# Optimization experiments

Measured on AMD Instinct MI355X. Metric: run time of the kernel, lower is better.

Reference implementation:

```python
import jax, jax.numpy as jnp
import numpy as np

N = 100_000      # nodes
E = 1_600_000    # edges
F_IN = 128       # n_features == conv_dim1..3
F_OUT = 256      # concat_dim
G = 2000         # number of graphs in the batch
EPS = 1e-5       # BatchNorm eps


def _xavier(k, shape):
    fan_in, fan_out = shape[-2], shape[-1]
    lim = float(np.sqrt(6.0 / (fan_in + fan_out)))
    return jax.random.uniform(k, shape, jnp.float32, -lim, lim)


def setup_inputs() -> dict:
    key = jax.random.key(0)
    ks = jax.random.split(key, 8)
    x = jax.random.normal(ks[0], (N, F_IN), jnp.float32)
    edge_index = jax.random.randint(ks[1], (2, E), 0, N, dtype=jnp.int64)
    batch = jnp.sort(jax.random.randint(ks[2], (N,), 0, G, dtype=jnp.int64))
    # layers 1..5: F_IN -> F_IN (stacked), layer 6: F_IN -> F_OUT
    Wi = _xavier(ks[3], (5, F_IN, F_IN))   # ARMA init_weight per layer
    Wr = _xavier(ks[4], (5, F_IN, F_IN))   # ARMA root_weight per layer
    b = jnp.zeros((5, F_IN), jnp.float32)  # ARMA bias per layer
    g = jnp.ones((5, F_IN), jnp.float32)   # BN gamma
    be = jnp.zeros((5, F_IN), jnp.float32) # BN beta
    Wi6 = _xavier(ks[5], (F_IN, F_OUT))
    Wr6 = _xavier(ks[6], (F_IN, F_OUT))
    b6 = jnp.zeros((F_OUT,), jnp.float32)
    g6 = jnp.ones((F_OUT,), jnp.float32)
    be6 = jnp.zeros((F_OUT,), jnp.float32)
    return dict(x=x, edge_index=edge_index, batch=batch, Wi=Wi, Wr=Wr, b=b,
                g=g, be=be, Wi6=Wi6, Wr6=Wr6, b6=b6, g6=g6, be6=be6)


def _arma(x, norm, row, col, Wi_l, Wr_l, b_l):
    # ARMAConv (num_stacks=1, num_layers=1, act=ReLU):
    #   out = ReLU( A_norm @ (x W_init) + x W_root + b )
    h = x @ Wi_l                                           # [N, F_out]
    msg = h[row] * norm[:, None]                           # gather + scale, [E, F_out]
    agg = jax.ops.segment_sum(msg, col, num_segments=N)    # scatter-add
    return jax.nn.relu(agg + x @ Wr_l + b_l)


def _bn(x, gamma, beta):
    # BatchNorm1d, training mode (biased batch variance)
    mu = x.mean(axis=0)
    var = x.var(axis=0)
    return gamma * (x - mu) * jax.lax.rsqrt(var + EPS) + beta


def reference(x, edge_index, batch, Wi, Wr, b, g, be, Wi6, Wr6, b6, g6, be6):
    row, col = edge_index[0], edge_index[1]
    # gcn_norm without self loops: D^-1/2 A D^-1/2 edge weights
    deg = jax.ops.segment_sum(jnp.ones((E,), x.dtype), col, num_segments=N)
    dinv = jnp.where(deg > 0, jax.lax.rsqrt(deg), 0.0)
    norm = dinv[row] * dinv[col]                           # [E]

    h = x
    for l in range(5):  # fixed small layer count
        h = _arma(h, norm, row, col, Wi[l], Wr[l], b[l])   # outer F.relu is idempotent
        h = _bn(h, g[l], be[l])
    h = _arma(h, norm, row, col, Wi6, Wr6, b6)
    h = _bn(h, g6, be6)
    # global_add_pool over graph ids; dropout = identity (deterministic baseline)
    out = jax.ops.segment_sum(h, batch, num_segments=G)    # [G, F_OUT]
    return out
```

## Files before the change

kernel.cpp:

```cpp
#include <hip/hip_runtime.h>

#define Nn 100000
#define NP 100001
#define Ee 1600000
#define Gg 2000
#define EPSf 1e-5f

typedef unsigned short ushort_t;
typedef __attribute__((ext_vector_type(8))) short short8;
typedef __attribute__((ext_vector_type(4))) float f32x4;
typedef __attribute__((ext_vector_type(4))) unsigned u32x4;

__device__ inline float bf2f(unsigned int u) {
    union { unsigned int i; float f; } v; v.i = u << 16; return v.f;
}
__device__ inline unsigned short f2bf(float f) {
    unsigned int x = __float_as_uint(f);
    unsigned int r = (x + 0x7fffu + ((x >> 16) & 1u)) >> 16;
    return (unsigned short)r;
}
__device__ inline int ldidx(const void* a, int i, int i64) {
    return i64 ? (int)((const long long*)a)[i] : ((const int*)a)[i];
}
__device__ inline float ldflt(const void* p, long long i, int f32) {
    return f32 ? ((const float*)p)[i] : bf2f(((const ushort_t*)p)[i]);
}


__global__ void k_flags(const void* gones, const void* ei, int* flags) {
    if (threadIdx.x == 0 && blockIdx.x == 0) {
        unsigned w = *(const unsigned*)gones;
        flags[0] = (w == 0x3F800000u) ? 1 : 0;
        const int* e = (const int*)ei;
        int nz = 0;
        for (int i = 0; i < 256; i++) nz |= e[2 * i + 1];
        flags[1] = nz ? 0 : 1;
    }
}


__global__ void k_hist(const void* __restrict__ ei, int* __restrict__ deg, const int* __restrict__ flags) {
    int i = blockIdx.x * 256 + threadIdx.x;
    if (i < Ee) {
        int c = ldidx(ei, Ee + i, flags[1]);
        atomicAdd(&deg[c], 1);
    }
}

__global__ void k_dinv(const int* __restrict__ deg, float* __restrict__ dinv) {
    int i = blockIdx.x * 256 + threadIdx.x;
    if (i < Nn) { int d = deg[i]; dinv[i] = d > 0 ? rsqrtf((float)d) : 0.f; }
}

__global__ void k_scan1(const int* __restrict__ deg, int* __restrict__ off, int* __restrict__ part) {
    __shared__ int sh[1024];
    int i = blockIdx.x * 1024 + threadIdx.x;
    int v = (i < Nn) ? ((deg[i] + 3) & ~3) : 0;
    sh[threadIdx.x] = v;
    __syncthreads();
    for (int ofs = 1; ofs < 1024; ofs <<= 1) {
        int t = 0;
        if ((int)threadIdx.x >= ofs) t = sh[threadIdx.x - ofs];
        __syncthreads();
        sh[threadIdx.x] += t;
        __syncthreads();
    }
    if (i < Nn) off[i] = sh[threadIdx.x] - v;
    if (threadIdx.x == 1023) part[blockIdx.x] = sh[1023];
}

__global__ void k_scan2(int* part, int nb) {
    if (threadIdx.x == 0 && blockIdx.x == 0) {
        int run = 0;
        for (int i = 0; i < nb; i++) { int t = part[i]; part[i] = run; run += t; }
        part[nb] = run;
    }
}

__global__ void k_scan3(int* __restrict__ off, const int* __restrict__ part, int* __restrict__ cursor) {
    int i = blockIdx.x * 256 + threadIdx.x;
    if (i < Nn) {
        int v = off[i] + part[i >> 10];
        off[i] = v;
        cursor[i] = v;
    }
    if (i == 0) off[Nn] = part[98];
}

__global__ void k_fillp(const void* __restrict__ ei, int* __restrict__ cursor,
                        int* __restrict__ srcS, const int* __restrict__ flags) {
    int range = blockIdx.x & 7;
    int e = (blockIdx.x >> 3) * 256 + threadIdx.x;
    if (e < Ee) {
        int i64 = flags[1];
        int c = ldidx(ei, Ee + e, i64);
        if (c >= range * 12500 && c < (range + 1) * 12500) {
            int r = ldidx(ei, e, i64);
            int p = atomicAdd(&cursor[c], 1);
            srcS[p] = r;
        }
    }
}

__global__ void k_pad(const int* __restrict__ cursor, const int* __restrict__ off,
                      int* __restrict__ srcS) {
    int i = blockIdx.x * 256 + threadIdx.x;
    if (i < Nn) {
        int e = off[i + 1];
        for (int p = cursor[i]; p < e; p++) srcS[p] = Nn;
    }
}

__global__ void k_zrow(ushort_t* __restrict__ Hi) {
    int t = threadIdx.x;
    int fc = t >> 4, j = t & 15;
    Hi[((size_t)fc * NP + Nn) * 16 + j] = 0;
}

__global__ void k_cvtp(const void* b, const void* b6, const void* g, const void* g6,
                       const void* be, const void* be6,
                       float* __restrict__ biasF, float* __restrict__ gF,
                       float* __restrict__ beF, const int* __restrict__ flags) {
    int i = blockIdx.x * 256 + threadIdx.x;
    if (i >= 2688) return;
    int grp = i / 896, r = i - grp * 896;
    int f32 = flags[0];
    const void* srcs[6] = { b, b6, g, g6, be, be6 };
    float* dsts[3] = { biasF, gF, beF };
    const void* s = (r < 640) ? srcs[grp * 2] : srcs[grp * 2 + 1];
    int idx = (r < 640) ? r : r - 640;
    dsts[grp][r] = ldflt(s, idx, f32);
}

__global__ void k_cvtx(const void* __restrict__ x, ushort_t* __restrict__ xq, const int* __restrict__ flags) {
    int node = blockIdx.x * 256 + threadIdx.x;
    int fc = blockIdx.y;
    if (node < Nn) {
        union { ushort_t u[16]; u32x4 v[2]; } t;
        if (flags[0]) {
            const float* p = (const float*)x + (size_t)node * 128 + fc * 16;
#pragma unroll
            for (int j = 0; j < 16; j++) t.u[j] = f2bf(p[j]);
        } else {
            const ushort_t* p = (const ushort_t*)x + (size_t)node * 128 + fc * 16;
#pragma unroll
            for (int j = 0; j < 16; j++) t.u[j] = p[j];
        }
        u32x4* d = (u32x4*)(xq + ((size_t)fc * Nn + node) * 16);
        d[0] = t.v[0]; d[1] = t.v[1];
    }
}

__global__ void k_pack(const void* __restrict__ Wi, const void* __restrict__ Wr,
                       const void* __restrict__ Wi6, const void* __restrict__ Wr6,
                       ushort_t* __restrict__ Bp, const int* __restrict__ flags) {
    int idx = blockIdx.x * 256 + threadIdx.x;
    if (idx >= 229376) return;
    int f32 = flags[0];
    if (idx < 163840) {
        int l = idx / 32768, rem = idx - l * 32768;
        int kg = rem / 2048, rem2 = rem - kg * 2048;
        int n = rem2 / 8, j = rem2 - n * 8;
        int k = kg * 8 + j;
        float v = (n < 128) ? ldflt(Wi, (l * 128 + k) * 128 + n, f32)
                            : ldflt(Wr, (l * 128 + k) * 128 + (n - 128), f32);
        Bp[idx] = f2bf(v);
    } else {
        int idx2 = idx - 163840;
        int kg = idx2 / 4096, rem2 = idx2 - kg * 4096;
        int n = rem2 / 8, j = rem2 - n * 8;
        int k = kg * 8 + j;
        float v = (n < 256) ? ldflt(Wi6, k * 256 + n, f32) : ldflt(Wr6, k * 256 + (n - 256), f32);
        Bp[idx] = f2bf(v);
    }
}

__global__ void k_fold(const ushort_t* __restrict__ Bp, const float* __restrict__ stat,
                       const float* __restrict__ gamma, const float* __restrict__ beta,
                       const float* __restrict__ bias,
                       ushort_t* __restrict__ Bp2, float* __restrict__ hcorr, int ncat) {
    __shared__ float red[128];
    int n = blockIdx.x, k = threadIdx.x;
    int fhalf = ncat >> 1;
    float mu = stat[k] * (1.f / Nn);
    float var = stat[128 + k] * (1.f / Nn) - mu * mu;
    float rs = rsqrtf(var + EPSf);
    float s = gamma[k] * rs;
    float h = beta[k] - s * mu;
    size_t idx = ((size_t)(k >> 3) * ncat + n) * 8 + (k & 7);
    float w = bf2f(Bp[idx]);
    Bp2[idx] = f2bf(w * s);
    red[k] = h * w;
    __syncthreads();
    for (int m = 64; m > 0; m >>= 1) { if (k < m) red[k] += red[k + m]; __syncthreads(); }
    if (k == 0) hcorr[n] = red[0] + (n >= fhalf ? bias[n - fhalf] : 0.f);
}

__global__ void k_h0(const float* __restrict__ bias, float* __restrict__ hc, int ncat) {
    int n = blockIdx.x * 256 + threadIdx.x;
    if (n < ncat) hc[n] = n >= (ncat >> 1) ? bias[n - (ncat >> 1)] : 0.f;
}


__global__ __launch_bounds__(256) void k_gemm(
        const ushort_t* __restrict__ Aq,
        const ushort_t* __restrict__ Bp, const float* __restrict__ hcorr,
        const float* __restrict__ dinv,
        ushort_t* __restrict__ Hi, ushort_t* __restrict__ yq, int ncat) {
    __shared__ ushort_t As[8448];
    const int tid = threadIdx.x, lane = tid & 63, wid = tid >> 6;
    const int row0 = blockIdx.x * 64;
    const int fhalf = ncat >> 1;

    {
        int node = row0 + lane;
#pragma unroll
        for (int i = 0; i < 4; i++) {
            int kg = wid * 4 + i;
            short8 t;
            if (node < Nn)
                t = *(const short8*)(Aq + ((size_t)(kg >> 1) * Nn + node) * 16 + (kg & 1) * 8);
            else {
#pragma unroll
                for (int j = 0; j < 8; j++) ((ushort_t*)&t)[j] = 0;
            }
            *(short8*)&As[(kg * 64 + lane) * 8] = t;
        }
    }
    __syncthreads();

    const int q = lane >> 4, l15 = lane & 15;
    const int wcL = wid * 64;

    f32x4 acc[4][4];
    f32x4 z; z.x = 0.f; z.y = 0.f; z.z = 0.f; z.w = 0.f;
#pragma unroll
    for (int rt = 0; rt < 4; rt++)
#pragma unroll
        for (int ct = 0; ct < 4; ct++) acc[rt][ct] = z;

#pragma unroll
    for (int kk = 0; kk < 4; kk++) {
        short8 af[4], bfr[4];
        int kg = kk * 4 + q;
#pragma unroll
        for (int rt = 0; rt < 4; rt++)
            af[rt] = *(const short8*)&As[((kg * 64) + rt * 16 + l15) * 8];
#pragma unroll
        for (int ct = 0; ct < 4; ct++) {
            int n = blockIdx.y * 256 + wcL + ct * 16 + l15;
            bfr[ct] = *(const short8*)(Bp + ((size_t)kg * ncat + n) * 8);
        }
#pragma unroll
        for (int rt = 0; rt < 4; rt++)
#pragma unroll
            for (int ct = 0; ct < 4; ct++)
                acc[rt][ct] = __builtin_amdgcn_mfma_f32_16x16x32_bf16(af[rt], bfr[ct], acc[rt][ct], 0, 0, 0);
    }

    ushort_t* stage = As;
#pragma unroll
    for (int half = 0; half < 2; half++) {
        __syncthreads();
#pragma unroll
        for (int ct = 0; ct < 4; ct++) {
            int lcol = wcL + ct * 16 + l15;
            int gcol = blockIdx.y * 256 + lcol;
            float hc = hcorr[gcol];
            bool isHi = gcol < fhalf;
#pragma unroll
            for (int rt2 = 0; rt2 < 2; rt2++) {
                int rt = half * 2 + rt2;
#pragma unroll
                for (int r = 0; r < 4; r++) {
                    int grow = row0 + rt * 16 + q * 4 + r;
                    int gr = grow < Nn ? grow : 0;
                    float v = acc[rt][ct][r] + hc;
                    if (isHi) v *= dinv[gr];
                    stage[(rt2 * 16 + q * 4 + r) * 264 + lcol] = f2bf(v);
                }
            }
        }
        __syncthreads();
        for (int chunk = tid; chunk < 512; chunk += 256) {
            int cg = chunk & 15, rl = chunk >> 4;
            int node = row0 + half * 32 + rl;
            if (node < Nn) {
                int gc0 = blockIdx.y * 256 + cg * 16;
                const u32x4* sp = (const u32x4*)&stage[rl * 264 + cg * 16];
                u32x4 v0 = sp[0], v1 = sp[1];
                ushort_t* dst = (gc0 < fhalf)
                    ? Hi + ((size_t)(gc0 >> 4) * NP + node) * 16
                    : yq + ((size_t)((gc0 - fhalf) >> 4) * Nn + node) * 16;
                u32x4* dp = (u32x4*)dst;
                dp[0] = v0; dp[1] = v1;
            }
        }
    }
}


__global__ __launch_bounds__(256) void k_agg8(const int* __restrict__ off, const int* __restrict__ src,
                                              const float* __restrict__ dinv, const unsigned* __restrict__ Hi2,
                                              unsigned* __restrict__ yq, float* __restrict__ stat,
                                              int F, int fcbase) {
    const int tid = threadIdx.x;
    const int w = tid >> 6, lane = tid & 63;
    const int sub = lane >> 3, fl = lane & 7;
    const int fc = fcbase + (blockIdx.x & 7);
    const int T = blockIdx.x >> 3;
    const unsigned* __restrict__ base = Hi2 + (size_t)fc * (NP * 8) + fl;
    float st0 = 0.f, st1 = 0.f, st2 = 0.f, st3 = 0.f;

#pragma unroll
    for (int pass = 0; pass < 4; pass++) {
        int node = T * 128 + pass * 32 + w * 8 + sub;
        bool valid = node < Nn;
        int p0 = 0, p1 = 0;
        if (valid) { p0 = off[node]; p1 = off[node + 1]; }
        float a0 = 0.f, a1 = 0.f;
        int p = p0;
        for (; p + 7 < p1; p += 8) {
            int4 sv0 = *(const int4*)(src + p);
            int4 sv1 = *(const int4*)(src + p + 4);
            unsigned u0 = base[(unsigned)sv0.x * 8u];
            unsigned u1 = base[(unsigned)sv0.y * 8u];
            unsigned u2 = base[(unsigned)sv0.z * 8u];
            unsigned u3 = base[(unsigned)sv0.w * 8u];
            unsigned u4 = base[(unsigned)sv1.x * 8u];
            unsigned u5 = base[(unsigned)sv1.y * 8u];
            unsigned u6 = base[(unsigned)sv1.z * 8u];
            unsigned u7 = base[(unsigned)sv1.w * 8u];
            a0 += bf2f(u0 & 0xffffu); a1 += bf2f(u0 >> 16);
            a0 += bf2f(u1 & 0xffffu); a1 += bf2f(u1 >> 16);
            a0 += bf2f(u2 & 0xffffu); a1 += bf2f(u2 >> 16);
            a0 += bf2f(u3 & 0xffffu); a1 += bf2f(u3 >> 16);
            a0 += bf2f(u4 & 0xffffu); a1 += bf2f(u4 >> 16);
            a0 += bf2f(u5 & 0xffffu); a1 += bf2f(u5 >> 16);
            a0 += bf2f(u6 & 0xffffu); a1 += bf2f(u6 >> 16);
            a0 += bf2f(u7 & 0xffffu); a1 += bf2f(u7 >> 16);
        }
        if (p < p1) {
            int4 sv0 = *(const int4*)(src + p);
            unsigned u0 = base[(unsigned)sv0.x * 8u];
            unsigned u1 = base[(unsigned)sv0.y * 8u];
            unsigned u2 = base[(unsigned)sv0.z * 8u];
            unsigned u3 = base[(unsigned)sv0.w * 8u];
            a0 += bf2f(u0 & 0xffffu); a1 += bf2f(u0 >> 16);
            a0 += bf2f(u1 & 0xffffu); a1 += bf2f(u1 >> 16);
            a0 += bf2f(u2 & 0xffffu); a1 += bf2f(u2 >> 16);
            a0 += bf2f(u3 & 0xffffu); a1 += bf2f(u3 >> 16);
        }
        if (valid) {
            float dv = dinv[node];
            unsigned* yp = yq + ((size_t)fc * Nn + node) * 8 + fl;
            unsigned uv = *yp;
            float vx = fmaxf(bf2f(uv & 0xffffu) + dv * a0, 0.f);
            float vy = fmaxf(bf2f(uv >> 16) + dv * a1, 0.f);
            *yp = (unsigned)f2bf(vx) | ((unsigned)f2bf(vy) << 16);
            st0 += vx; st1 += vx * vx;
            st2 += vy; st3 += vy * vy;
        }
    }
#pragma unroll
    for (int m = 8; m <= 32; m <<= 1) {
        st0 += __shfl_xor(st0, m, 64);
        st1 += __shfl_xor(st1, m, 64);
        st2 += __shfl_xor(st2, m, 64);
        st3 += __shfl_xor(st3, m, 64);
    }
    __shared__ float red[4][8][4];
    if (sub == 0) {
        red[w][fl][0] = st0; red[w][fl][1] = st1;
        red[w][fl][2] = st2; red[w][fl][3] = st3;
    }
    __syncthreads();
    if (tid < 32) {
        int rfl = tid >> 2, k = tid & 3;
        float s = red[0][rfl][k] + red[1][rfl][k] + red[2][rfl][k] + red[3][rfl][k];
        int f = fc * 16 + rfl * 2 + (k >> 1);
        atomicAdd(&stat[(k & 1) * F + f], s);
    }
}


__device__ inline int lb(const void* a, int n, int key, int i64) {
    int lo = 0, hi = n;
    while (lo < hi) { int mid = (lo + hi) >> 1; if (ldidx(a, mid, i64) < key) lo = mid + 1; else hi = mid; }
    return lo;
}

__global__ void k_pool(const ushort_t* __restrict__ y6q, const float* __restrict__ stat,
                       const float* __restrict__ g6, const float* __restrict__ be6,
                       const void* __restrict__ batch, void* __restrict__ out,
                       const int* __restrict__ flags) {
    int g = blockIdx.x;
    int f = threadIdx.x;
    int i64 = flags[1];
    int start = lb(batch, Nn, g, i64);
    int end = lb(batch, Nn, g + 1, i64);
    const ushort_t* yp = y6q + (size_t)(f >> 4) * Nn * 16 + (f & 15);
    float s = 0.f;
    for (int n = start; n < end; n++) s += bf2f(yp[(size_t)n * 16]);
    int cnt = end - start;
    float mu = stat[f] * (1.f / Nn);
    float var = stat[256 + f] * (1.f / Nn) - mu * mu;
    float rs = rsqrtf(var + EPSf);
    float val = g6[f] * rs * (s - (float)cnt * mu) + (float)cnt * be6[f];
    if (flags[0]) ((float*)out)[(size_t)g * 256 + f] = val;
    else          ((ushort_t*)out)[(size_t)g * 256 + f] = f2bf(val);
}


extern "C" void kernel_launch(void* const* d_in, const int* in_sizes, int n_in,
                              void* d_out, int out_size, void* d_ws, size_t ws_size,
                              hipStream_t stream) {
    const void* x    = d_in[0];
    const void* ei   = d_in[1];
    const void* batch= d_in[2];
    const void* Wi   = d_in[3];
    const void* Wr   = d_in[4];
    const void* b    = d_in[5];
    const void* g    = d_in[6];
    const void* be   = d_in[7];
    const void* Wi6  = d_in[8];
    const void* Wr6  = d_in[9];
    const void* b6   = d_in[10];
    const void* g6   = d_in[11];
    const void* be6  = d_in[12];

    char* p = (char*)d_ws;
    auto alloc = [&](size_t bytes) { char* r = p; p += (bytes + 511) & ~(size_t)511; return r; };
    ushort_t* HiB  = (ushort_t*)alloc((size_t)NP * 256 * 2);
    ushort_t* xq   = (ushort_t*)alloc((size_t)Nn * 128 * 2);
    ushort_t* yAq  = (ushort_t*)alloc((size_t)Nn * 128 * 2);
    ushort_t* yBq  = (ushort_t*)alloc((size_t)Nn * 128 * 2);
    ushort_t* y6q  = (ushort_t*)alloc((size_t)Nn * 256 * 2);
    int* srcS      = (int*)alloc(((size_t)Ee + 4 * Nn + 64) * 4);
    int* off       = (int*)alloc((size_t)(Nn + 1) * 4);
    int* cursor    = (int*)alloc((size_t)Nn * 4);
    int* deg       = (int*)alloc((size_t)Nn * 4);
    float* dinv    = (float*)alloc((size_t)Nn * 4);
    int* part      = (int*)alloc(128 * 4);
    float* statsA  = (float*)alloc(6 * 512 * 4);
    ushort_t* Bp   = (ushort_t*)alloc(229376 * 2);
    ushort_t* Bp2  = (ushort_t*)alloc(65536 * 2);
    float* hcorrA  = (float*)alloc(512 * 4);
    int* flags     = (int*)alloc(2 * 4);
    float* biasF   = (float*)alloc(896 * 4);
    float* gF      = (float*)alloc(896 * 4);
    float* beF     = (float*)alloc(896 * 4);
    const unsigned* Hi2 = (const unsigned*)HiB;

    const int AGG_GRID = 782 * 8;

    k_flags<<<1, 64, 0, stream>>>(g, ei, flags);
    k_cvtp<<<11, 256, 0, stream>>>(b, b6, g, g6, be, be6, biasF, gF, beF, flags);

    hipMemsetAsync(deg, 0, (size_t)Nn * 4, stream);
    hipMemsetAsync(statsA, 0, 6 * 512 * 4, stream);
    k_hist<<<6250, 256, 0, stream>>>(ei, deg, flags);
    k_dinv<<<391, 256, 0, stream>>>(deg, dinv);
    k_scan1<<<98, 1024, 0, stream>>>(deg, off, part);
    k_scan2<<<1, 64, 0, stream>>>(part, 98);
    k_scan3<<<391, 256, 0, stream>>>(off, part, cursor);
    k_fillp<<<50000, 256, 0, stream>>>(ei, cursor, srcS, flags);
    k_pad<<<391, 256, 0, stream>>>(cursor, off, srcS);
    k_zrow<<<1, 256, 0, stream>>>(HiB);
    k_pack<<<896, 256, 0, stream>>>(Wi, Wr, Wi6, Wr6, Bp, flags);
    k_cvtx<<<dim3(391, 8), 256, 0, stream>>>(x, xq, flags);
    k_h0<<<1, 256, 0, stream>>>(biasF, hcorrA, 256);

    k_gemm<<<dim3(1563, 1), 256, 0, stream>>>(xq, Bp, hcorrA, dinv, HiB, yAq, 256);
    k_agg8<<<AGG_GRID, 256, 0, stream>>>(off, srcS, dinv, Hi2, (unsigned*)yAq, statsA, 128, 0);
    k_fold<<<256, 128, 0, stream>>>(Bp + 32768, statsA, gF, beF, biasF + 128, Bp2, hcorrA, 256);

    k_gemm<<<dim3(1563, 1), 256, 0, stream>>>(yAq, Bp2, hcorrA, dinv, HiB, yBq, 256);
    k_agg8<<<AGG_GRID, 256, 0, stream>>>(off, srcS, dinv, Hi2, (unsigned*)yBq, statsA + 512, 128, 0);
    k_fold<<<256, 128, 0, stream>>>(Bp + 65536, statsA + 512, gF + 128, beF + 128, biasF + 256, Bp2, hcorrA, 256);

    k_gemm<<<dim3(1563, 1), 256, 0, stream>>>(yBq, Bp2, hcorrA, dinv, HiB, yAq, 256);
    k_agg8<<<AGG_GRID, 256, 0, stream>>>(off, srcS, dinv, Hi2, (unsigned*)yAq, statsA + 1024, 128, 0);
    k_fold<<<256, 128, 0, stream>>>(Bp + 98304, statsA + 1024, gF + 256, beF + 256, biasF + 384, Bp2, hcorrA, 256);

    k_gemm<<<dim3(1563, 1), 256, 0, stream>>>(yAq, Bp2, hcorrA, dinv, HiB, yBq, 256);
    k_agg8<<<AGG_GRID, 256, 0, stream>>>(off, srcS, dinv, Hi2, (unsigned*)yBq, statsA + 1536, 128, 0);
    k_fold<<<256, 128, 0, stream>>>(Bp + 131072, statsA + 1536, gF + 384, beF + 384, biasF + 512, Bp2, hcorrA, 256);

    k_gemm<<<dim3(1563, 1), 256, 0, stream>>>(yBq, Bp2, hcorrA, dinv, HiB, yAq, 256);
    k_agg8<<<AGG_GRID, 256, 0, stream>>>(off, srcS, dinv, Hi2, (unsigned*)yAq, statsA + 2048, 128, 0);
    k_fold<<<512, 128, 0, stream>>>(Bp + 163840, statsA + 2048, gF + 512, beF + 512, biasF + 640, Bp2, hcorrA, 512);

    k_gemm<<<dim3(1563, 2), 256, 0, stream>>>(yAq, Bp2, hcorrA, dinv, HiB, y6q, 512);
    k_agg8<<<AGG_GRID, 256, 0, stream>>>(off, srcS, dinv, Hi2, (unsigned*)y6q, statsA + 2560, 256, 0);
    k_agg8<<<AGG_GRID, 256, 0, stream>>>(off, srcS, dinv, Hi2, (unsigned*)y6q, statsA + 2560, 256, 8);
    k_pool<<<Gg, 256, 0, stream>>>(y6q, statsA + 2560, gF + 640, beF + 640, batch, d_out, flags);
}
```

Baseline: 1.165 ms.

## Make GEMM persistent over row tiles with register-resident B, unroll aggregation loop

```diff
diff --git a/kernel.cpp b/kernel.cpp
--- a/kernel.cpp
+++ b/kernel.cpp
@@ -207,93 +207,87 @@
         const ushort_t* __restrict__ Bp, const float* __restrict__ hcorr,
         const float* __restrict__ dinv,
         ushort_t* __restrict__ Hi, ushort_t* __restrict__ yq, int ncat) {
-    __shared__ ushort_t As[8448];
+    __shared__ ushort_t stage[32 * 264];
     const int tid = threadIdx.x, lane = tid & 63, wid = tid >> 6;
-    const int row0 = blockIdx.x * 64;
+    const int q = lane >> 4, l15 = lane & 15;
     const int fhalf = ncat >> 1;
-
-    {
-        int node = row0 + lane;
-#pragma unroll
-        for (int i = 0; i < 4; i++) {
-            int kg = wid * 4 + i;
-            short8 t;
-            if (node < Nn)
-                t = *(const short8*)(Aq + ((size_t)(kg >> 1) * Nn + node) * 16 + (kg & 1) * 8);
-            else {
-#pragma unroll
-                for (int j = 0; j < 8; j++) ((ushort_t*)&t)[j] = 0;
+    const int colW = blockIdx.y * 256 + wid * 64;
+
+    short8 bfr[4][4];
+    float hc[4];
+#pragma unroll
+    for (int kk = 0; kk < 4; kk++) {
+        int kg = kk * 4 + q;
+#pragma unroll
+        for (int ct = 0; ct < 4; ct++)
+            bfr[kk][ct] = *(const short8*)(Bp + ((size_t)kg * ncat + colW + ct * 16 + l15) * 8);
+    }
+#pragma unroll
+    for (int ct = 0; ct < 4; ct++) hc[ct] = hcorr[colW + ct * 16 + l15];
+
+    for (int t = 0; t < 4; t++) {
+        int row0 = (blockIdx.x * 4 + t) * 64;
+        if (row0 >= Nn) break;
+
+        f32x4 acc[4][4];
+        f32x4 z; z.x = 0.f; z.y = 0.f; z.z = 0.f; z.w = 0.f;
+#pragma unroll
+        for (int rt = 0; rt < 4; rt++)
+#pragma unroll
+            for (int ct = 0; ct < 4; ct++) acc[rt][ct] = z;
+
+#pragma unroll
+        for (int kk = 0; kk < 4; kk++) {
+            int kg = kk * 4 + q;
+            const ushort_t* ap = Aq + (size_t)(kg >> 1) * Nn * 16 + (kg & 1) * 8;
+            short8 af[4];
+#pragma unroll
+            for (int rt = 0; rt < 4; rt++) {
+                int node = row0 + rt * 16 + l15;
+                if (node >= Nn) node = Nn - 1;
+                af[rt] = *(const short8*)(ap + (size_t)node * 16);
             }
-            *(short8*)&As[(kg * 64 + lane) * 8] = t;
-        }
-    }
-    __syncthreads();
-
-    const int q = lane >> 4, l15 = lane & 15;
-    const int wcL = wid * 64;
-
-    f32x4 acc[4][4];
-    f32x4 z; z.x = 0.f; z.y = 0.f; z.z = 0.f; z.w = 0.f;
-#pragma unroll
-    for (int rt = 0; rt < 4; rt++)
-#pragma unroll
-        for (int ct = 0; ct < 4; ct++) acc[rt][ct] = z;
-
-#pragma unroll
-    for (int kk = 0; kk < 4; kk++) {
-        short8 af[4], bfr[4];
-        int kg = kk * 4 + q;
-#pragma unroll
-        for (int rt = 0; rt < 4; rt++)
-            af[rt] = *(const short8*)&As[((kg * 64) + rt * 16 + l15) * 8];
-#pragma unroll
-        for (int ct = 0; ct < 4; ct++) {
-            int n = blockIdx.y * 256 + wcL + ct * 16 + l15;
-            bfr[ct] = *(const short8*)(Bp + ((size_t)kg * ncat + n) * 8);
-        }
-#pragma unroll
-        for (int rt = 0; rt < 4; rt++)
-#pragma unroll
-            for (int ct = 0; ct < 4; ct++)
-                acc[rt][ct] = __builtin_amdgcn_mfma_f32_16x16x32_bf16(af[rt], bfr[ct], acc[rt][ct], 0, 0, 0);
-    }
-
-    ushort_t* stage = As;
-#pragma unroll
-    for (int half = 0; half < 2; half++) {
-        __syncthreads();
-#pragma unroll
-        for (int ct = 0; ct < 4; ct++) {
-            int lcol = wcL + ct * 16 + l15;
-            int gcol = blockIdx.y * 256 + lcol;
-            float hc = hcorr[gcol];
-            bool isHi = gcol < fhalf;
-#pragma unroll
-            for (int rt2 = 0; rt2 < 2; rt2++) {
-                int rt = half * 2 + rt2;
-#pragma unroll
-                for (int r = 0; r < 4; r++) {
-                    int grow = row0 + rt * 16 + q * 4 + r;
-                    int gr = grow < Nn ? grow : 0;
-                    float v = acc[rt][ct][r] + hc;
-                    if (isHi) v *= dinv[gr];
-                    stage[(rt2 * 16 + q * 4 + r) * 264 + lcol] = f2bf(v);
+#pragma unroll
+            for (int rt = 0; rt < 4; rt++)
+#pragma unroll
+                for (int ct = 0; ct < 4; ct++)
+                    acc[rt][ct] = __builtin_amdgcn_mfma_f32_16x16x32_bf16(af[rt], bfr[kk][ct], acc[rt][ct], 0, 0, 0);
+        }
+
+#pragma unroll
+        for (int half = 0; half < 2; half++) {
+            __syncthreads();
+#pragma unroll
+            for (int ct = 0; ct < 4; ct++) {
+                int lcol = wid * 64 + ct * 16 + l15;
+                bool isHi = (blockIdx.y * 256 + lcol) < fhalf;
+#pragma unroll
+                for (int rt2 = 0; rt2 < 2; rt2++) {
+                    int rt = half * 2 + rt2;
+#pragma unroll
+                    for (int r = 0; r < 4; r++) {
+                        int grow = row0 + rt * 16 + q * 4 + r;
+                        int gr = grow < Nn ? grow : 0;
+                        float v = acc[rt][ct][r] + hc[ct];
+                        if (isHi) v *= dinv[gr];
+                        stage[(rt2 * 16 + q * 4 + r) * 264 + lcol] = f2bf(v);
+                    }
                 }
             }
-        }
-        __syncthreads();
-        for (int chunk = tid; chunk < 512; chunk += 256) {
-            int cg = chunk & 15, rl = chunk >> 4;
-            int node = row0 + half * 32 + rl;
-            if (node < Nn) {
-                int gc0 = blockIdx.y * 256 + cg * 16;
-                const u32x4* sp = (const u32x4*)&stage[rl * 264 + cg * 16];
-                u32x4 v0 = sp[0], v1 = sp[1];
-                ushort_t* dst = (gc0 < fhalf)
-                    ? Hi + ((size_t)(gc0 >> 4) * NP + node) * 16
-                    : yq + ((size_t)((gc0 - fhalf) >> 4) * Nn + node) * 16;
-                u32x4* dp = (u32x4*)dst;
-                dp[0] = v0; dp[1] = v1;
+            __syncthreads();
+            for (int chunk = tid; chunk < 512; chunk += 256) {
+                int cg = chunk & 15, rl = chunk >> 4;
+                int node = row0 + half * 32 + rl;
+                if (node < Nn) {
+                    int gc0 = blockIdx.y * 256 + cg * 16;
+                    const u32x4* sp = (const u32x4*)&stage[rl * 264 + cg * 16];
+                    u32x4 v0 = sp[0], v1 = sp[1];
+                    ushort_t* dst = (gc0 < fhalf)
+                        ? Hi + ((size_t)(gc0 >> 4) * NP + node) * 16
+                        : yq + ((size_t)((gc0 - fhalf) >> 4) * Nn + node) * 16;
+                    u32x4* dp = (u32x4*)dst;
+                    dp[0] = v0; dp[1] = v1;
+                }
             }
         }
     }
@@ -320,17 +314,27 @@
         if (valid) { p0 = off[node]; p1 = off[node + 1]; }
         float a0 = 0.f, a1 = 0.f;
         int p = p0;
-        for (; p + 7 < p1; p += 8) {
-            int4 sv0 = *(const int4*)(src + p);
-            int4 sv1 = *(const int4*)(src + p + 4);
-            unsigned u0 = base[(unsigned)sv0.x * 8u];
-            unsigned u1 = base[(unsigned)sv0.y * 8u];
-            unsigned u2 = base[(unsigned)sv0.z * 8u];
-            unsigned u3 = base[(unsigned)sv0.w * 8u];
-            unsigned u4 = base[(unsigned)sv1.x * 8u];
-            unsigned u5 = base[(unsigned)sv1.y * 8u];
-            unsigned u6 = base[(unsigned)sv1.z * 8u];
-            unsigned u7 = base[(unsigned)sv1.w * 8u];
+        for (; p + 15 < p1; p += 16) {
+            int4 sa = *(const int4*)(src + p);
+            int4 sb = *(const int4*)(src + p + 4);
+            int4 sc = *(const int4*)(src + p + 8);
+            int4 sd = *(const int4*)(src + p + 12);
+            unsigned u0 = base[(unsigned)sa.x * 8u];
+            unsigned u1 = base[(unsigned)sa.y * 8u];
+            unsigned u2 = base[(unsigned)sa.z * 8u];
+            unsigned u3 = base[(unsigned)sa.w * 8u];
+            unsigned u4 = base[(unsigned)sb.x * 8u];
+            unsigned u5 = base[(unsigned)sb.y * 8u];
+            unsigned u6 = base[(unsigned)sb.z * 8u];
+            unsigned u7 = base[(unsigned)sb.w * 8u];
+            unsigned u8 = base[(unsigned)sc.x * 8u];
+            unsigned u9 = base[(unsigned)sc.y * 8u];
+            unsigned uA = base[(unsigned)sc.z * 8u];
+            unsigned uB = base[(unsigned)sc.w * 8u];
+            unsigned uC = base[(unsigned)sd.x * 8u];
+            unsigned uD = base[(unsigned)sd.y * 8u];
+            unsigned uE = base[(unsigned)sd.z * 8u];
+            unsigned uF = base[(unsigned)sd.w * 8u];
             a0 += bf2f(u0 & 0xffffu); a1 += bf2f(u0 >> 16);
             a0 += bf2f(u1 & 0xffffu); a1 += bf2f(u1 >> 16);
             a0 += bf2f(u2 & 0xffffu); a1 += bf2f(u2 >> 16);
@@ -339,13 +343,41 @@
             a0 += bf2f(u5 & 0xffffu); a1 += bf2f(u5 >> 16);
             a0 += bf2f(u6 & 0xffffu); a1 += bf2f(u6 >> 16);
             a0 += bf2f(u7 & 0xffffu); a1 += bf2f(u7 >> 16);
+            a0 += bf2f(u8 & 0xffffu); a1 += bf2f(u8 >> 16);
+            a0 += bf2f(u9 & 0xffffu); a1 += bf2f(u9 >> 16);
+            a0 += bf2f(uA & 0xffffu); a1 += bf2f(uA >> 16);
+            a0 += bf2f(uB & 0xffffu); a1 += bf2f(uB >> 16);
+            a0 += bf2f(uC & 0xffffu); a1 += bf2f(uC >> 16);
+            a0 += bf2f(uD & 0xffffu); a1 += bf2f(uD >> 16);
+            a0 += bf2f(uE & 0xffffu); a1 += bf2f(uE >> 16);
+            a0 += bf2f(uF & 0xffffu); a1 += bf2f(uF >> 16);
+        }
+        for (; p + 7 < p1; p += 8) {
+            int4 sa = *(const int4*)(src + p);
+            int4 sb = *(const int4*)(src + p + 4);
+            unsigned u0 = base[(unsigned)sa.x * 8u];
+            unsigned u1 = base[(unsigned)sa.y * 8u];
+            unsigned u2 = base[(unsigned)sa.z * 8u];
+            unsigned u3 = base[(unsigned)sa.w * 8u];
+            unsigned u4 = base[(unsigned)sb.x * 8u];
+            unsigned u5 = base[(unsigned)sb.y * 8u];
+            unsigned u6 = base[(unsigned)sb.z * 8u];
+            unsigned u7 = base[(unsigned)sb.w * 8u];
+            a0 += bf2f(u0 & 0xffffu); a1 += bf2f(u0 >> 16);
+            a0 += bf2f(u1 & 0xffffu); a1 += bf2f(u1 >> 16);
+            a0 += bf2f(u2 & 0xffffu); a1 += bf2f(u2 >> 16);
+            a0 += bf2f(u3 & 0xffffu); a1 += bf2f(u3 >> 16);
+            a0 += bf2f(u4 & 0xffffu); a1 += bf2f(u4 >> 16);
+            a0 += bf2f(u5 & 0xffffu); a1 += bf2f(u5 >> 16);
+            a0 += bf2f(u6 & 0xffffu); a1 += bf2f(u6 >> 16);
+            a0 += bf2f(u7 & 0xffffu); a1 += bf2f(u7 >> 16);
         }
         if (p < p1) {
-            int4 sv0 = *(const int4*)(src + p);
-            unsigned u0 = base[(unsigned)sv0.x * 8u];
-            unsigned u1 = base[(unsigned)sv0.y * 8u];
-            unsigned u2 = base[(unsigned)sv0.z * 8u];
-            unsigned u3 = base[(unsigned)sv0.w * 8u];
+            int4 sa = *(const int4*)(src + p);
+            unsigned u0 = base[(unsigned)sa.x * 8u];
+            unsigned u1 = base[(unsigned)sa.y * 8u];
+            unsigned u2 = base[(unsigned)sa.z * 8u];
+            unsigned u3 = base[(unsigned)sa.w * 8u];
             a0 += bf2f(u0 & 0xffffu); a1 += bf2f(u0 >> 16);
             a0 += bf2f(u1 & 0xffffu); a1 += bf2f(u1 >> 16);
             a0 += bf2f(u2 & 0xffffu); a1 += bf2f(u2 >> 16);
@@ -453,6 +485,7 @@
     const unsigned* Hi2 = (const unsigned*)HiB;
 
     const int AGG_GRID = 782 * 8;
+    const int GEMM_GRID = 391;
 
     k_flags<<<1, 64, 0, stream>>>(g, ei, flags);
     k_cvtp<<<11, 256, 0, stream>>>(b, b6, g, g6, be, be6, biasF, gF, beF, flags);
@@ -471,27 +504,27 @@
     k_cvtx<<<dim3(391, 8), 256, 0, stream>>>(x, xq, flags);
     k_h0<<<1, 256, 0, stream>>>(biasF, hcorrA, 256);
 
-    k_gemm<<<dim3(1563, 1), 256, 0, stream>>>(xq, Bp, hcorrA, dinv, HiB, yAq, 256);
+    k_gemm<<<dim3(GEMM_GRID, 1), 256, 0, stream>>>(xq, Bp, hcorrA, dinv, HiB, yAq, 256);
     k_agg8<<<AGG_GRID, 256, 0, stream>>>(off, srcS, dinv, Hi2, (unsigned*)yAq, statsA, 128, 0);
     k_fold<<<256, 128, 0, stream>>>(Bp + 32768, statsA, gF, beF, biasF + 128, Bp2, hcorrA, 256);
 
-    k_gemm<<<dim3(1563, 1), 256, 0, stream>>>(yAq, Bp2, hcorrA, dinv, HiB, yBq, 256);
+    k_gemm<<<dim3(GEMM_GRID, 1), 256, 0, stream>>>(yAq, Bp2, hcorrA, dinv, HiB, yBq, 256);
     k_agg8<<<AGG_GRID, 256, 0, stream>>>(off, srcS, dinv, Hi2, (unsigned*)yBq, statsA + 512, 128, 0);
     k_fold<<<256, 128, 0, stream>>>(Bp + 65536, statsA + 512, gF + 128, beF + 128, biasF + 256, Bp2, hcorrA, 256);
 
-    k_gemm<<<dim3(1563, 1), 256, 0, stream>>>(yBq, Bp2, hcorrA, dinv, HiB, yAq, 256);
+    k_gemm<<<dim3(GEMM_GRID, 1), 256, 0, stream>>>(yBq, Bp2, hcorrA, dinv, HiB, yAq, 256);
     k_agg8<<<AGG_GRID, 256, 0, stream>>>(off, srcS, dinv, Hi2, (unsigned*)yAq, statsA + 1024, 128, 0);
     k_fold<<<256, 128, 0, stream>>>(Bp + 98304, statsA + 1024, gF + 256, beF + 256, biasF + 384, Bp2, hcorrA, 256);
 
-    k_gemm<<<dim3(1563, 1), 256, 0, stream>>>(yAq, Bp2, hcorrA, dinv, HiB, yBq, 256);
+    k_gemm<<<dim3(GEMM_GRID, 1), 256, 0, stream>>>(yAq, Bp2, hcorrA, dinv, HiB, yBq, 256);
     k_agg8<<<AGG_GRID, 256, 0, stream>>>(off, srcS, dinv, Hi2, (unsigned*)yBq, statsA + 1536, 128, 0);
     k_fold<<<256, 128, 0, stream>>>(Bp + 131072, statsA + 1536, gF + 384, beF + 384, biasF + 512, Bp2, hcorrA, 256);
 
-    k_gemm<<<dim3(1563, 1), 256, 0, stream>>>(yBq, Bp2, hcorrA, dinv, HiB, yAq, 256);
+    k_gemm<<<dim3(GEMM_GRID, 1), 256, 0, stream>>>(yBq, Bp2, hcorrA, dinv, HiB, yAq, 256);
     k_agg8<<<AGG_GRID, 256, 0, stream>>>(off, srcS, dinv, Hi2, (unsigned*)yAq, statsA + 2048, 128, 0);
     k_fold<<<512, 128, 0, stream>>>(Bp + 163840, statsA + 2048, gF + 512, beF + 512, biasF + 640, Bp2, hcorrA, 512);
 
-    k_gemm<<<dim3(1563, 2), 256, 0, stream>>>(yAq, Bp2, hcorrA, dinv, HiB, y6q, 512);
+    k_gemm<<<dim3(GEMM_GRID, 2), 256, 0, stream>>>(yAq, Bp2, hcorrA, dinv, HiB, y6q, 512);
     k_agg8<<<AGG_GRID, 256, 0, stream>>>(off, srcS, dinv, Hi2, (unsigned*)y6q, statsA + 2560, 256, 0);
     k_agg8<<<AGG_GRID, 256, 0, stream>>>(off, srcS, dinv, Hi2, (unsigned*)y6q, statsA + 2560, 256, 8);
     k_pool<<<Gg, 256, 0, stream>>>(y6q, statsA + 2560, gF + 640, beF + 640, batch, d_out, flags);
```

New measurement: 1.244 ms. +6.8%, slower.
